# Kernel optimization log

Hardware: AMD Instinct MI355X
Metric: run time of the kernel (lower is better)

Reference implementation:

```python
import jax, jax.numpy as jnp
import numpy as np

N_RAYS = 16384
MAX_STEPS = 512          # fixed march-step budget per ray (dense-padded packed samples)
GRID_R = 128             # occupancy grid resolution
NEAR = 0.05
FAR = 3.0
STEP = (FAR - NEAR) / MAX_STEPS   # render_step_size


def setup_inputs() -> dict:
    key = jax.random.key(0)
    k1, k2, k3 = jax.random.split(key, 3)
    rays_o = jax.random.uniform(k1, (N_RAYS, 3), minval=-0.5, maxval=0.5, dtype=jnp.float32)
    d = jax.random.normal(k2, (N_RAYS, 3), dtype=jnp.float32)
    rays_d = d / jnp.linalg.norm(d, axis=-1, keepdims=True)
    aabb = jnp.array([[-1.0, -1.0, -1.0], [1.0, 1.0, 1.0]], dtype=jnp.float32)
    occ_grid = jax.random.bernoulli(k3, 0.3, (GRID_R, GRID_R, GRID_R))  # bool occupancy
    return {"rays_o": rays_o, "rays_d": rays_d, "aabb": aabb, "occ_grid": occ_grid}


def reference(rays_o, rays_d, aabb, occ_grid):
    # --- ray / AABB intersection (per-ray valid t interval) ---
    safe_d = jnp.where(jnp.abs(rays_d) > 1e-10, rays_d, 1e-10)
    inv_d = 1.0 / safe_d
    t0 = (aabb[0] - rays_o) * inv_d          # [N,3]
    t1 = (aabb[1] - rays_o) * inv_d
    tmin = jnp.maximum(jnp.max(jnp.minimum(t0, t1), axis=-1), NEAR)   # [N]
    tmax = jnp.minimum(jnp.min(jnp.maximum(t0, t1), axis=-1), FAR)    # [N]

    # --- uniform marching bins (cone_angle = 0) ---
    edges = NEAR + jnp.arange(MAX_STEPS + 1, dtype=rays_o.dtype) * STEP
    starts = edges[:-1]                      # [S]
    ends = edges[1:]                         # [S]
    mids = 0.5 * (starts + ends)             # [S]

    # sample midpoint positions: [N,S,3]
    pos = rays_o[:, None, :] + rays_d[:, None, :] * mids[None, :, None]

    # --- occupancy-grid lookup (irregular gather) ---
    scale = (pos - aabb[0]) / (aabb[1] - aabb[0])          # [N,S,3] in [0,1) if inside
    idx = jnp.clip((scale * GRID_R).astype(jnp.int32), 0, GRID_R - 1)
    occ = occ_grid[idx[..., 0], idx[..., 1], idx[..., 2]]  # [N,S] bool
    inside = jnp.all((scale >= 0.0) & (scale < 1.0), axis=-1)

    valid = (starts[None, :] >= tmin[:, None]) & (ends[None, :] <= tmax[:, None]) & occ & inside  # [N,S]

    # --- packed_info (exclusive cumsum of per-ray counts) ---
    counts = valid.sum(axis=1).astype(jnp.int32)            # [N]
    offsets = jnp.concatenate([jnp.zeros((1,), jnp.int32), jnp.cumsum(counts)[:-1].astype(jnp.int32)])
    packed_info = jnp.stack([offsets, counts], axis=1)      # [N,2]

    # --- unpack_info equivalent: per-sample ray index, then irregular gather ---
    ray_indices = jnp.broadcast_to(jnp.arange(N_RAYS, dtype=jnp.int32)[:, None],
                                   (N_RAYS, MAX_STEPS)).reshape(-1)  # [N*S]
    mask = valid.reshape(-1)                                 # [N*S]
    maskf = mask.astype(rays_o.dtype)[:, None]

    origins = rays_o[ray_indices] * maskf                    # [N*S,3]
    dirs = rays_d[ray_indices] * maskf                       # [N*S,3]
    s_flat = jnp.where(mask, jnp.broadcast_to(starts, (N_RAYS, MAX_STEPS)).reshape(-1), 0.0)
    e_flat = jnp.where(mask, jnp.broadcast_to(ends, (N_RAYS, MAX_STEPS)).reshape(-1), 0.0)

    return origins, dirs, s_flat, e_flat, packed_info, ray_indices, mask
```

## Files before the change

### kernel.cpp

```cpp
#include <hip/hip_runtime.h>

#define N_RAYS 16384
#define MAX_STEPS 512
#define GRID_R 128
#define N_CELLS (GRID_R * GRID_R * GRID_R)
#define NS (N_RAYS * MAX_STEPS)

typedef float vfloat4 __attribute__((ext_vector_type(4)));

#define WS_COUNTS_OFF 1024
#define WS_BITS_OFF 131072
#define WS_NEEDED (WS_BITS_OFF + N_CELLS / 8)

__global__ __launch_bounds__(256)
void pack_occ(const void* __restrict__ occ, unsigned long long* __restrict__ bits) {
    const int* pi = (const int*)occ;
    const float* pf = (const float*)occ;
    bool oki = true, okf = true;
#pragma unroll
    for (int k = 0; k < 4; ++k) {
        const int w = threadIdx.x * 4 + k;
        const int v = pi[w];
        oki = oki && (v == 0 || v == 1);
        const float f = pf[w];
        okf = okf && (f == 0.0f || f == 1.0f);
    }
    oki = __all(oki); okf = __all(okf);
    __shared__ int s_oki[4], s_okf[4];
    if ((threadIdx.x & 63) == 0) { s_oki[threadIdx.x >> 6] = oki; s_okf[threadIdx.x >> 6] = okf; }
    __syncthreads();
    const bool all_i = s_oki[0] && s_oki[1] && s_oki[2] && s_oki[3];
    const bool all_f = s_okf[0] && s_okf[1] && s_okf[2] && s_okf[3];
    const int mode = all_i ? 0 : (all_f ? 1 : 2);

    const int idx = blockIdx.x * 256 + threadIdx.x;
    bool v;
    if (mode == 0)      v = pi[idx] != 0;
    else if (mode == 1) v = pf[idx] != 0.0f;
    else                v = ((const unsigned char*)occ)[idx] != 0;
    const unsigned long long b = __ballot(v);
    if ((threadIdx.x & 63) == 0) bits[idx >> 6] = b;
}

__global__ __launch_bounds__(512)
void sample_kernel(const float* __restrict__ rays_o, const float* __restrict__ rays_d,
                   const float* __restrict__ aabb,
                   const unsigned int* __restrict__ bits,
                   float* __restrict__ out, int* __restrict__ counts)
{
    const int r = blockIdx.x;
    const int s = threadIdx.x;

    const float ox = rays_o[3 * r + 0], oy = rays_o[3 * r + 1], oz = rays_o[3 * r + 2];
    const float dx = rays_d[3 * r + 0], dy = rays_d[3 * r + 1], dz = rays_d[3 * r + 2];
    const float a0x = aabb[0], a0y = aabb[1], a0z = aabb[2];
    const float a1x = aabb[3], a1y = aabb[4], a1z = aabb[5];

    const float sdx = (fabsf(dx) > 1e-10f) ? dx : 1e-10f;
    const float sdy = (fabsf(dy) > 1e-10f) ? dy : 1e-10f;
    const float sdz = (fabsf(dz) > 1e-10f) ? dz : 1e-10f;
    const float invx = __fdiv_rn(1.0f, sdx);
    const float invy = __fdiv_rn(1.0f, sdy);
    const float invz = __fdiv_rn(1.0f, sdz);

    const float t0x = __fmul_rn(__fsub_rn(a0x, ox), invx);
    const float t1x = __fmul_rn(__fsub_rn(a1x, ox), invx);
    const float t0y = __fmul_rn(__fsub_rn(a0y, oy), invy);
    const float t1y = __fmul_rn(__fsub_rn(a1y, oy), invy);
    const float t0z = __fmul_rn(__fsub_rn(a0z, oz), invz);
    const float t1z = __fmul_rn(__fsub_rn(a1z, oz), invz);

    const float tmin = fmaxf(fmaxf(fmaxf(fminf(t0x, t1x), fminf(t0y, t1y)), fminf(t0z, t1z)), 0.05f);
    const float tmax = fminf(fminf(fminf(fmaxf(t0x, t1x), fmaxf(t0y, t1y)), fmaxf(t0z, t1z)), 3.0f);

    const float step_f = (float)((3.0 - 0.05) / 512.0);
    const float start = __fadd_rn(0.05f, __fmul_rn((float)s, step_f));
    const float end   = __fadd_rn(0.05f, __fmul_rn((float)(s + 1), step_f));
    const float mid   = __fmul_rn(0.5f, __fadd_rn(start, end));

    const float px = __fadd_rn(ox, __fmul_rn(dx, mid));
    const float py = __fadd_rn(oy, __fmul_rn(dy, mid));
    const float pz = __fadd_rn(oz, __fmul_rn(dz, mid));

    const float scx = __fdiv_rn(__fsub_rn(px, a0x), __fsub_rn(a1x, a0x));
    const float scy = __fdiv_rn(__fsub_rn(py, a0y), __fsub_rn(a1y, a0y));
    const float scz = __fdiv_rn(__fsub_rn(pz, a0z), __fsub_rn(a1z, a0z));

    const bool inside = (scx >= 0.0f) && (scx < 1.0f) &&
                        (scy >= 0.0f) && (scy < 1.0f) &&
                        (scz >= 0.0f) && (scz < 1.0f);
    const bool geom = inside && (start >= tmin) && (end <= tmax);

    bool valid = false;
    if (geom) {
        int gx = (int)__fmul_rn(scx, (float)GRID_R);
        int gy = (int)__fmul_rn(scy, (float)GRID_R);
        int gz = (int)__fmul_rn(scz, (float)GRID_R);
        gx = min(max(gx, 0), GRID_R - 1);
        gy = min(max(gy, 0), GRID_R - 1);
        gz = min(max(gz, 0), GRID_R - 1);
        const int lin = (gx * GRID_R + gy) * GRID_R + gz;
        valid = (bits[lin >> 5] >> (lin & 31)) & 1u;
    }

    __shared__ unsigned long long wmask[8];
    const unsigned long long b = __ballot(valid);
    if ((s & 63) == 0) wmask[s >> 6] = b;
    __syncthreads();

#define MASK_BIT(smp) ((wmask[(smp) >> 6] >> ((smp) & 63)) & 1ull)

    if (s < 384) {
        const int f = 4 * s;
        vfloat4 vo, vd;
#pragma unroll
        for (int k = 0; k < 4; ++k) {
            const int ff = f + k;
            const int smp = ff / 3;
            const int c = ff - smp * 3;
            const bool m = MASK_BIT(smp);
            const float oc = (c == 0) ? ox : ((c == 1) ? oy : oz);
            const float dc = (c == 0) ? dx : ((c == 1) ? dy : dz);
            vo[k] = m ? oc : 0.0f;
            vd[k] = m ? dc : 0.0f;
        }
        ((vfloat4*)out)[(long)r * 384 + s] = vo;
        ((vfloat4*)(out + 3L * NS))[(long)r * 384 + s] = vd;
    }

    {
        const int grp = s >> 7;
        const int t = s & 127;
        vfloat4 v;
#pragma unroll
        for (int k = 0; k < 4; ++k) {
            const int smp = 4 * t + k;
            const bool m = MASK_BIT(smp);
            float val;
            if (grp == 0)      val = m ? __fadd_rn(0.05f, __fmul_rn((float)smp, step_f)) : 0.0f;
            else if (grp == 1) val = m ? __fadd_rn(0.05f, __fmul_rn((float)(smp + 1), step_f)) : 0.0f;
            else if (grp == 2) val = (float)r;
            else               val = m ? 1.0f : 0.0f;
            v[k] = val;
        }
        float* basep;
        if (grp == 0)      basep = out + 6L * NS;
        else if (grp == 1) basep = out + 7L * NS;
        else if (grp == 2) basep = out + 8L * NS + 2L * N_RAYS;
        else               basep = out + 8L * NS + 2L * N_RAYS + (long)NS;
        ((vfloat4*)basep)[(long)r * 128 + t] = v;
    }
#undef MASK_BIT

    if (s == 0) {
        int t = 0;
#pragma unroll
        for (int w = 0; w < 8; ++w) t += __popcll(wmask[w]);
        counts[r] = t;
    }
}

__global__ __launch_bounds__(1024)
void scan_kernel(const int* __restrict__ counts, float* __restrict__ packed)
{
    __shared__ int partial[1024];
    const int tid = threadIdx.x;
    const int base = tid * 16;
    int sum = 0;
#pragma unroll
    for (int i = 0; i < 16; ++i) sum += counts[base + i];
    partial[tid] = sum;
    __syncthreads();
    for (int off = 1; off < 1024; off <<= 1) {
        int v = (tid >= off) ? partial[tid - off] : 0;
        __syncthreads();
        partial[tid] += v;
        __syncthreads();
    }
    int run = (tid == 0) ? 0 : partial[tid - 1];
#pragma unroll
    for (int i = 0; i < 16; ++i) {
        const int c = counts[base + i];
        packed[2 * (base + i) + 0] = (float)run;
        packed[2 * (base + i) + 1] = (float)c;
        run += c;
    }
}

__global__ void detect_dtype(const void* __restrict__ occ, int* __restrict__ flag) {
    __shared__ int ok_int, ok_flt;
    if (threadIdx.x == 0) { ok_int = 1; ok_flt = 1; }
    __syncthreads();
    const int*   pi = (const int*)occ;
    const float* pf = (const float*)occ;
    for (int i = threadIdx.x; i < 1024; i += blockDim.x) {
        int v = pi[i];
        if (v != 0 && v != 1) atomicAnd(&ok_int, 0);
        float f = pf[i];
        if (!(f == 0.0f || f == 1.0f)) atomicAnd(&ok_flt, 0);
    }
    __syncthreads();
    if (threadIdx.x == 0) flag[0] = ok_int ? 0 : (ok_flt ? 1 : 2);
}

__global__ __launch_bounds__(512)
void sample_fallback(const float* __restrict__ rays_o, const float* __restrict__ rays_d,
                     const float* __restrict__ aabb, const void* __restrict__ occ,
                     const int* __restrict__ flag_p, float* __restrict__ out,
                     int* __restrict__ counts)
{
    const int r = blockIdx.x;
    const int s = threadIdx.x;
    const int mode = flag_p[0];
    const float ox = rays_o[3 * r + 0], oy = rays_o[3 * r + 1], oz = rays_o[3 * r + 2];
    const float dx = rays_d[3 * r + 0], dy = rays_d[3 * r + 1], dz = rays_d[3 * r + 2];
    const float a0x = aabb[0], a0y = aabb[1], a0z = aabb[2];
    const float a1x = aabb[3], a1y = aabb[4], a1z = aabb[5];
    const float sdx = (fabsf(dx) > 1e-10f) ? dx : 1e-10f;
    const float sdy = (fabsf(dy) > 1e-10f) ? dy : 1e-10f;
    const float sdz = (fabsf(dz) > 1e-10f) ? dz : 1e-10f;
    const float invx = __fdiv_rn(1.0f, sdx);
    const float invy = __fdiv_rn(1.0f, sdy);
    const float invz = __fdiv_rn(1.0f, sdz);
    const float t0x = __fmul_rn(__fsub_rn(a0x, ox), invx);
    const float t1x = __fmul_rn(__fsub_rn(a1x, ox), invx);
    const float t0y = __fmul_rn(__fsub_rn(a0y, oy), invy);
    const float t1y = __fmul_rn(__fsub_rn(a1y, oy), invy);
    const float t0z = __fmul_rn(__fsub_rn(a0z, oz), invz);
    const float t1z = __fmul_rn(__fsub_rn(a1z, oz), invz);
    const float tmin = fmaxf(fmaxf(fmaxf(fminf(t0x, t1x), fminf(t0y, t1y)), fminf(t0z, t1z)), 0.05f);
    const float tmax = fminf(fminf(fminf(fmaxf(t0x, t1x), fmaxf(t0y, t1y)), fmaxf(t0z, t1z)), 3.0f);
    const float step_f = (float)((3.0 - 0.05) / 512.0);
    const float start = __fadd_rn(0.05f, __fmul_rn((float)s, step_f));
    const float end   = __fadd_rn(0.05f, __fmul_rn((float)(s + 1), step_f));
    const float mid   = __fmul_rn(0.5f, __fadd_rn(start, end));
    const float px = __fadd_rn(ox, __fmul_rn(dx, mid));
    const float py = __fadd_rn(oy, __fmul_rn(dy, mid));
    const float pz = __fadd_rn(oz, __fmul_rn(dz, mid));
    const float scx = __fdiv_rn(__fsub_rn(px, a0x), __fsub_rn(a1x, a0x));
    const float scy = __fdiv_rn(__fsub_rn(py, a0y), __fsub_rn(a1y, a0y));
    const float scz = __fdiv_rn(__fsub_rn(pz, a0z), __fsub_rn(a1z, a0z));
    const bool inside = (scx >= 0.0f) && (scx < 1.0f) &&
                        (scy >= 0.0f) && (scy < 1.0f) &&
                        (scz >= 0.0f) && (scz < 1.0f);
    const bool geom = inside && (start >= tmin) && (end <= tmax);
    bool valid = false;
    if (geom) {
        int gx = (int)__fmul_rn(scx, (float)GRID_R);
        int gy = (int)__fmul_rn(scy, (float)GRID_R);
        int gz = (int)__fmul_rn(scz, (float)GRID_R);
        gx = min(max(gx, 0), GRID_R - 1);
        gy = min(max(gy, 0), GRID_R - 1);
        gz = min(max(gz, 0), GRID_R - 1);
        const int lin = (gx * GRID_R + gy) * GRID_R + gz;
        if (mode == 0)      valid = ((const int*)occ)[lin] != 0;
        else if (mode == 1) valid = ((const float*)occ)[lin] != 0.0f;
        else                valid = ((const unsigned char*)occ)[lin] != 0;
    }
    const int i = (r << 9) | s;
    float* og = out;
    float* dr = out + 3L * NS;
    float* sf = out + 6L * NS;
    float* ef = out + 7L * NS;
    float* ri = out + 8L * NS + 2L * N_RAYS;
    float* mk = ri + (long)NS;
    og[3 * i + 0] = valid ? ox : 0.0f;
    og[3 * i + 1] = valid ? oy : 0.0f;
    og[3 * i + 2] = valid ? oz : 0.0f;
    dr[3 * i + 0] = valid ? dx : 0.0f;
    dr[3 * i + 1] = valid ? dy : 0.0f;
    dr[3 * i + 2] = valid ? dz : 0.0f;
    sf[i] = valid ? start : 0.0f;
    ef[i] = valid ? end : 0.0f;
    ri[i] = (float)r;
    mk[i] = valid ? 1.0f : 0.0f;
    const unsigned long long b = __ballot(valid);
    __shared__ int wcount[8];
    if ((threadIdx.x & 63) == 0) wcount[threadIdx.x >> 6] = __popcll(b);
    __syncthreads();
    if (threadIdx.x == 0) {
        int t = 0;
#pragma unroll
        for (int w = 0; w < 8; ++w) t += wcount[w];
        counts[r] = t;
    }
}

extern "C" void kernel_launch(void* const* d_in, const int* in_sizes, int n_in,
                              void* d_out, int out_size, void* d_ws, size_t ws_size,
                              hipStream_t stream) {
    const float* rays_o = (const float*)d_in[0];
    const float* rays_d = (const float*)d_in[1];
    const float* aabb   = (const float*)d_in[2];
    const void*  occ    = d_in[3];
    float* out = (float*)d_out;

    int* counts = (int*)((char*)d_ws + WS_COUNTS_OFF);

    if (ws_size >= (size_t)WS_NEEDED) {
        unsigned long long* bits64 = (unsigned long long*)((char*)d_ws + WS_BITS_OFF);
        pack_occ<<<N_CELLS / 256, 256, 0, stream>>>(occ, bits64);
        sample_kernel<<<N_RAYS, 512, 0, stream>>>(rays_o, rays_d, aabb,
                                                  (const unsigned int*)bits64,
                                                  out, counts);
    } else {
        int* flag = (int*)d_ws;
        detect_dtype<<<1, 256, 0, stream>>>(occ, flag);
        sample_fallback<<<N_RAYS, 512, 0, stream>>>(rays_o, rays_d, aabb, occ, flag, out, counts);
    }
    scan_kernel<<<1, 1024, 0, stream>>>(counts, out + 8L * NS);
}
```

Before: 364.0 us.

## Use per-wave ballot masks for output writes and a wave-shuffle scan

The sample kernel no longer shares the ballot mask through shared memory behind a block barrier. Each wave writes the outputs for its own 64 samples directly from its ballot result, with the origin, direction, start, end, ray-index and mask stores split across lanes, so the barrier before the bulk stores goes away. The count reduction still takes one barrier, but only after the stores. The scan kernel replaces its log-step shared-memory scan, which had many barriers, with a wave shuffle scan plus per-wave totals, and uses vectorized int4 loads and float2 stores. The main risk is uneven lane utilization in the store phases.

Measured after the change: 406.0 us. +11.5%, slower.

```diff
diff --git a/kernel.cpp b/kernel.cpp
--- a/kernel.cpp
+++ b/kernel.cpp
@@ -7,6 +7,7 @@
 #define NS (N_RAYS * MAX_STEPS)
 
 typedef float vfloat4 __attribute__((ext_vector_type(4)));
+typedef float vfloat2 __attribute__((ext_vector_type(2)));
 
 #define WS_COUNTS_OFF 1024
 #define WS_BITS_OFF 131072
@@ -50,6 +51,8 @@
 {
     const int r = blockIdx.x;
     const int s = threadIdx.x;
+    const int wir = s >> 6;
+    const int lane = s & 63;
 
     const float ox = rays_o[3 * r + 0], oy = rays_o[3 * r + 1], oz = rays_o[3 * r + 2];
     const float dx = rays_d[3 * r + 0], dy = rays_d[3 * r + 1], dz = rays_d[3 * r + 2];
@@ -103,59 +106,74 @@
         valid = (bits[lin >> 5] >> (lin & 31)) & 1u;
     }
 
-    __shared__ unsigned long long wmask[8];
     const unsigned long long b = __ballot(valid);
-    if ((s & 63) == 0) wmask[s >> 6] = b;
-    __syncthreads();
-
-#define MASK_BIT(smp) ((wmask[(smp) >> 6] >> ((smp) & 63)) & 1ull)
-
-    if (s < 384) {
-        const int f = 4 * s;
-        vfloat4 vo, vd;
-#pragma unroll
-        for (int k = 0; k < 4; ++k) {
-            const int ff = f + k;
+
+    vfloat4* const f4 = (vfloat4*)out;
+    const long o_f4  = (long)r * 384 + wir * 48;
+    const long d_f4  = (3L * NS) / 4 + (long)r * 384 + wir * 48;
+    const long sf_f4 = (6L * NS) / 4 + (long)r * 128 + wir * 16;
+    const long ef_f4 = (7L * NS) / 4 + (long)r * 128 + wir * 16;
+    const long ri_f4 = (8L * NS + 2L * N_RAYS) / 4 + (long)r * 128 + wir * 16;
+    const long mk_f4 = ri_f4 + NS / 4;
+
+    const int step0 = wir * 64;
+
+    auto od_vec = [&](int k, bool dir) {
+        vfloat4 v;
+#pragma unroll
+        for (int j = 0; j < 4; ++j) {
+            const int ff = 4 * k + j;
             const int smp = ff / 3;
             const int c = ff - smp * 3;
-            const bool m = MASK_BIT(smp);
+            const bool m = (b >> smp) & 1ull;
             const float oc = (c == 0) ? ox : ((c == 1) ? oy : oz);
             const float dc = (c == 0) ? dx : ((c == 1) ? dy : dz);
-            vo[k] = m ? oc : 0.0f;
-            vd[k] = m ? dc : 0.0f;
+            v[j] = m ? (dir ? dc : oc) : 0.0f;
         }
-        ((vfloat4*)out)[(long)r * 384 + s] = vo;
-        ((vfloat4*)(out + 3L * NS))[(long)r * 384 + s] = vd;
-    }
-
-    {
-        const int grp = s >> 7;
-        const int t = s & 127;
+        return v;
+    };
+    auto se_vec = [&](int k, int plus) {
         vfloat4 v;
 #pragma unroll
-        for (int k = 0; k < 4; ++k) {
-            const int smp = 4 * t + k;
-            const bool m = MASK_BIT(smp);
-            float val;
-            if (grp == 0)      val = m ? __fadd_rn(0.05f, __fmul_rn((float)smp, step_f)) : 0.0f;
-            else if (grp == 1) val = m ? __fadd_rn(0.05f, __fmul_rn((float)(smp + 1), step_f)) : 0.0f;
-            else if (grp == 2) val = (float)r;
-            else               val = m ? 1.0f : 0.0f;
-            v[k] = val;
+        for (int j = 0; j < 4; ++j) {
+            const int smp = 4 * k + j;
+            const bool m = (b >> smp) & 1ull;
+            v[j] = m ? __fadd_rn(0.05f, __fmul_rn((float)(step0 + smp + plus), step_f)) : 0.0f;
         }
-        float* basep;
-        if (grp == 0)      basep = out + 6L * NS;
-        else if (grp == 1) basep = out + 7L * NS;
-        else if (grp == 2) basep = out + 8L * NS + 2L * N_RAYS;
-        else               basep = out + 8L * NS + 2L * N_RAYS + (long)NS;
-        ((vfloat4*)basep)[(long)r * 128 + t] = v;
-    }
-#undef MASK_BIT
-
+        return v;
+    };
+
+    if (lane < 48) {
+        f4[o_f4 + lane] = od_vec(lane, false);
+    } else {
+        f4[sf_f4 + (lane - 48)] = se_vec(lane - 48, 0);
+    }
+    if (lane < 48) {
+        f4[d_f4 + lane] = od_vec(lane, true);
+    } else {
+        f4[ef_f4 + (lane - 48)] = se_vec(lane - 48, 1);
+    }
+    if (lane < 16) {
+        vfloat4 v = {(float)r, (float)r, (float)r, (float)r};
+        f4[ri_f4 + lane] = v;
+    } else if (lane < 32) {
+        const int k = lane - 16;
+        vfloat4 v;
+#pragma unroll
+        for (int j = 0; j < 4; ++j) {
+            const int smp = 4 * k + j;
+            v[j] = ((b >> smp) & 1ull) ? 1.0f : 0.0f;
+        }
+        f4[mk_f4 + k] = v;
+    }
+
+    __shared__ int wcnt[8];
+    if (lane == 0) wcnt[wir] = __popcll(b);
+    __syncthreads();
     if (s == 0) {
         int t = 0;
 #pragma unroll
-        for (int w = 0; w < 8; ++w) t += __popcll(wmask[w]);
+        for (int w = 0; w < 8; ++w) t += wcnt[w];
         counts[r] = t;
     }
 }
@@ -163,27 +181,42 @@
 __global__ __launch_bounds__(1024)
 void scan_kernel(const int* __restrict__ counts, float* __restrict__ packed)
 {
-    __shared__ int partial[1024];
     const int tid = threadIdx.x;
+    const int lane = tid & 63;
+    const int w = tid >> 6;
     const int base = tid * 16;
-    int sum = 0;
-#pragma unroll
-    for (int i = 0; i < 16; ++i) sum += counts[base + i];
-    partial[tid] = sum;
-    __syncthreads();
-    for (int off = 1; off < 1024; off <<= 1) {
-        int v = (tid >= off) ? partial[tid - off] : 0;
-        __syncthreads();
-        partial[tid] += v;
-        __syncthreads();
-    }
-    int run = (tid == 0) ? 0 : partial[tid - 1];
+
+    int c[16];
+#pragma unroll
+    for (int i = 0; i < 16; i += 4) {
+        const int4 q = ((const int4*)counts)[(base + i) >> 2];
+        c[i + 0] = q.x; c[i + 1] = q.y; c[i + 2] = q.z; c[i + 3] = q.w;
+    }
+    int ts = 0;
+#pragma unroll
+    for (int i = 0; i < 16; ++i) ts += c[i];
+
+    int incl = ts;
+#pragma unroll
+    for (int off = 1; off < 64; off <<= 1) {
+        const int n = __shfl_up(incl, off);
+        if (lane >= off) incl += n;
+    }
+
+    __shared__ int wtot[16];
+    if (lane == 63) wtot[w] = incl;
+    __syncthreads();
+
+    int wbase = 0;
+#pragma unroll
+    for (int i = 0; i < 16; ++i) wbase += (i < w) ? wtot[i] : 0;
+
+    int run = wbase + (incl - ts);
 #pragma unroll
     for (int i = 0; i < 16; ++i) {
-        const int c = counts[base + i];
-        packed[2 * (base + i) + 0] = (float)run;
-        packed[2 * (base + i) + 1] = (float)c;
-        run += c;
+        vfloat2 v = {(float)run, (float)c[i]};
+        ((vfloat2*)packed)[base + i] = v;
+        run += c[i];
     }
 }
 
```
